# Performance work log

Hardware: AMD Instinct MI355X
Metric: run time of the kernel (lower is better)

The kernel has to match this reference:

```python
import jax, jax.numpy as jnp
import numpy as np

S = 10       # speakers (== num nodes N, per module construction)
D = 1024     # hidden_dim
R = 2 * S * S  # num_relations


def _forward(global_features, speaker, Wq, Wk, rgcn_weight, rgcn_root,
             rgcn_bias, gcn_rel_w, gcn_rel_b, gcn_root_w):
    N, d = global_features.shape
    # ---- single-head global attention -> edge weights (softmax over keys) ----
    # keys are the node features themselves (stacked N times in the original)
    q = global_features @ Wq                       # [N, D]
    k = global_features @ Wk                       # [N, D]
    attn = jax.nn.softmax((q @ k.T) / jnp.sqrt(jnp.asarray(d, q.dtype)), axis=-1)  # [N, N]

    # ---- dense all-pairs edge list, row-major (i, j) like itertools product ----
    src = jnp.repeat(jnp.arange(N), N)             # edge_index[0]
    dst = jnp.tile(jnp.arange(N), N)               # edge_index[1]
    edge_weight = attn.reshape(-1)                 # matches torch.flatten order

    # edge_type id = 2*(s_i*S + s_j) + direction, direction = 0 if i<j else 1
    etype = 2 * (speaker[src] * S + speaker[dst]) + (src >= dst).astype(speaker.dtype)

    # ---- RGCN with per-relation MEAN aggregation (PyG RGCNConv default) ----
    # mean is per (relation, dst-node) over weighted messages; transform is linear
    # so we fold weight[rel] into each edge and normalize by segment counts.
    seg = etype * N + dst                           # (relation, dst) segment id
    cnt = jax.ops.segment_sum(jnp.ones_like(edge_weight), seg, num_segments=R * N)
    w_e = edge_weight / cnt[seg]                    # cnt >= 1 on every live edge
    # per-edge gather of relation weight + matmul: [E, D] x [E, D, D] -> [E, D]
    msg = w_e[:, None] * jnp.einsum('ed,edf->ef', global_features[src], rgcn_weight[etype])
    out = jax.ops.segment_sum(msg, dst, num_segments=N)    # scatter-add to dst
    out = out + global_features @ rgcn_root + rgcn_bias    # root + bias

    # ---- GraphConv (sum aggregation, no edge weight): lin_rel(agg) + lin_root(x) ----
    agg = jax.ops.segment_sum(out[src], dst, num_segments=N)
    x2 = agg @ gcn_rel_w + gcn_rel_b + out @ gcn_root_w

    return jnp.concatenate([x2, global_features], axis=-1)  # [N, 2D]


def setup_inputs() -> dict:
    key = jax.random.key(0)
    ks = jax.random.split(key, 10)
    scale = 0.02
    return {
        'global_features': jax.random.normal(ks[0], (S, D), dtype=jnp.float32),
        'speaker': jax.random.randint(ks[1], (S,), 0, S, dtype=jnp.int32),
        'Wq': jax.random.normal(ks[2], (D, D), dtype=jnp.float32) * scale,
        'Wk': jax.random.normal(ks[3], (D, D), dtype=jnp.float32) * scale,
        'rgcn_weight': jax.random.normal(ks[4], (R, D, D), dtype=jnp.float32) * scale,
        'rgcn_root': jax.random.normal(ks[5], (D, D), dtype=jnp.float32) * scale,
        'rgcn_bias': jax.random.normal(ks[6], (D,), dtype=jnp.float32) * scale,
        'gcn_rel_w': jax.random.normal(ks[7], (D, D), dtype=jnp.float32) * scale,
        'gcn_rel_b': jax.random.normal(ks[8], (D,), dtype=jnp.float32) * scale,
        'gcn_root_w': jax.random.normal(ks[9], (D, D), dtype=jnp.float32) * scale,
    }


def reference(global_features, speaker, Wq, Wk, rgcn_weight, rgcn_root,
              rgcn_bias, gcn_rel_w, gcn_rel_b, gcn_root_w):
    return _forward(global_features, speaker, Wq, Wk, rgcn_weight, rgcn_root,
                    rgcn_bias, gcn_rel_w, gcn_rel_b, gcn_root_w)
```

## Files before the change

kernel.cpp:

```cpp
#include <hip/hip_runtime.h>

#define N 10
#define D 1024
#define NREL 200
#define KCH 32
#define KLEN 32
#define MAXG 8

typedef float f32x4 __attribute__((ext_vector_type(4)));

#define OFF_Q       0
#define OFF_K       (OFF_Q + N*D)
#define OFF_ROOT    (OFF_K + N*D)
#define OFF_X2ACC   (OFF_ROOT + N*D)
#define OFF_AGGREL  (OFF_X2ACC + N*D)
#define ZERO_FLOATS (OFF_AGGREL + D)
#define OFF_EM      ZERO_FLOATS
#define OFF_WE      (OFF_EM + N*N*D)
#define OFF_NITEMS  (OFF_WE + 128)
#define OFF_ITEMS   (OFF_NITEMS + 16)
#define OFF_EMPART  (OFF_ITEMS + 1024)

__global__ void build_groups(const int* __restrict__ speaker, int* __restrict__ n_items,
                             int* __restrict__ items) {
    __shared__ int sp[N];
    __shared__ int gcnt[NREL];
    __shared__ int ibase[NREL];
    int tid = threadIdx.x;
    if (tid < N) sp[tid] = speaker[tid];
    __syncthreads();
    if (tid < NREL) {
        int c = 0;
        for (int e = 0; e < N * N; ++e) {
            int src = e / N, dst = e % N;
            int et = 2 * (sp[src] * N + sp[dst]) + (src >= dst ? 1 : 0);
            c += (et == tid);
        }
        gcnt[tid] = c;
    }
    __syncthreads();
    if (tid == 0) {
        int b = 0;
        for (int t = 0; t < NREL; ++t) { ibase[t] = b; b += (gcnt[t] + MAXG - 1) / MAXG; }
        *n_items = b;
    }
    __syncthreads();
    if (tid < NREL && gcnt[tid] > 0) {
        int it = ibase[tid], slot = 0;
        int* rec = items + it * 10;
        for (int e = 0; e < N * N; ++e) {
            int src = e / N, dst = e % N;
            int et = 2 * (sp[src] * N + sp[dst]) + (src >= dst ? 1 : 0);
            if (et != tid) continue;
            if (slot == 0) rec[0] = tid;
            rec[2 + slot] = e;
            if (++slot == MAXG) { rec[1] = MAXG; ++it; rec = items + it * 10; slot = 0; }
        }
        if (slot > 0) { rec[1] = slot; for (int g = slot; g < MAXG; ++g) rec[2 + g] = -1; }
    }
}

__global__ void big_fused(const float* __restrict__ X, const float* __restrict__ Wrel,
                          const int* __restrict__ n_items, const int* __restrict__ items,
                          const float* __restrict__ Wq, const float* __restrict__ Wk,
                          const float* __restrict__ Wroot,
                          float* __restrict__ q, float* __restrict__ kout,
                          float* __restrict__ rootacc, float* __restrict__ em_part) {
    int bx = blockIdx.x, by = blockIdx.y, tid = threadIdx.x;
    if (bx < 100) {
        if (bx >= *n_items) return;
        __shared__ int   meta[10];
        __shared__ float xs[MAXG][KLEN];
        if (tid < 10) meta[tid] = items[bx * 10 + tid];
        __syncthreads();
        int t = meta[0], gsize = meta[1];
        {
            int g = tid >> 5, k = tid & 31;
            int e = meta[2 + g];
            xs[g][k] = (g < gsize) ? X[(e / N) * D + by * KLEN + k] : 0.f;
        }
        __syncthreads();
        int c0 = tid * 4;
        const float* W = Wrel + (size_t)t * D * D + (size_t)by * KLEN * D;
        f32x4 acc[MAXG];
#pragma unroll
        for (int g = 0; g < MAXG; ++g) acc[g] = 0.f;
#pragma unroll 4
        for (int k = 0; k < KLEN; ++k) {
            f32x4 w4 = *reinterpret_cast<const f32x4*>(W + (size_t)k * D + c0);
#pragma unroll
            for (int g = 0; g < MAXG; ++g) acc[g] += xs[g][k] * w4;
        }
        for (int g = 0; g < gsize; ++g) {
            *reinterpret_cast<f32x4*>(
                em_part + ((size_t)(by * (N * N) + meta[2 + g])) * D + c0) = acc[g];
        }
    } else {
        int sel = bx - 100;
        int kb  = (by & 7) * 128;
        int c   = (by >> 3) * 256 + tid;
        const float* W = (sel == 0) ? Wq : (sel == 1) ? Wk : Wroot;
        float*       Y = (sel == 0) ? q  : (sel == 1) ? kout : rootacc;
        __shared__ float xs2[N][128];
        for (int idx = tid; idx < N * 128; idx += 256) {
            int r = idx >> 7, k = idx & 127;
            xs2[r][k] = X[r * D + kb + k];
        }
        __syncthreads();
        float acc[N];
#pragma unroll
        for (int r = 0; r < N; ++r) acc[r] = 0.f;
#pragma unroll 4
        for (int k = 0; k < 128; ++k) {
            float w = W[(size_t)(kb + k) * D + c];
#pragma unroll
            for (int r = 0; r < N; ++r) acc[r] += xs2[r][k] * w;
        }
#pragma unroll
        for (int r = 0; r < N; ++r) atomicAdd(&Y[r * D + c], acc[r]);
    }
}

__global__ void reduce_em(const float* __restrict__ em_part, float* __restrict__ em) {
    __shared__ float ps[2][128];
    int e  = blockIdx.x;
    int c  = blockIdx.y * 128 + (threadIdx.x & 127);
    int h  = threadIdx.x >> 7;
    float s = 0.f;
#pragma unroll
    for (int i = 0; i < KCH / 2; ++i) {
        int by = h * (KCH / 2) + i;
        s += em_part[((size_t)(by * (N * N) + e)) * D + c];
    }
    ps[h][threadIdx.x & 127] = s;
    __syncthreads();
    if (threadIdx.x < 128) em[(size_t)e * D + c] = ps[0][threadIdx.x] + ps[1][threadIdx.x];
}

__global__ void attn_edges(const float* __restrict__ q, const float* __restrict__ k,
                           const int* __restrict__ speaker, float* __restrict__ w_e) {
    __shared__ float logits[N * N];
    __shared__ float attn[N * N];
    __shared__ int   cnt[NREL * N];
    int tid  = threadIdx.x;
    int wave = tid >> 6, lane = tid & 63;

    for (int p = wave; p < N * N; p += 16) {
        int i = p / N, j = p % N;
        const f32x4* qp = reinterpret_cast<const f32x4*>(q + i * D);
        const f32x4* kp = reinterpret_cast<const f32x4*>(k + j * D);
        float acc = 0.f;
#pragma unroll
        for (int it = 0; it < 4; ++it) {
            f32x4 qa = qp[lane + it * 64];
            f32x4 ka = kp[lane + it * 64];
            acc += qa.x * ka.x + qa.y * ka.y + qa.z * ka.z + qa.w * ka.w;
        }
        for (int off = 32; off; off >>= 1) acc += __shfl_down(acc, off);
        if (lane == 0) logits[p] = acc * (1.0f / 32.0f);
    }
    __syncthreads();

    if (tid < N) {
        float m = -1e30f;
        for (int j = 0; j < N; ++j) m = fmaxf(m, logits[tid * N + j]);
        float s = 0.f, e[N];
        for (int j = 0; j < N; ++j) { e[j] = expf(logits[tid * N + j] - m); s += e[j]; }
        for (int j = 0; j < N; ++j) attn[tid * N + j] = e[j] / s;
    }
    for (int i = tid; i < NREL * N; i += 1024) cnt[i] = 0;
    __syncthreads();

    int et = 0;
    if (tid < N * N) {
        int src = tid / N, dst = tid % N;
        et = 2 * (speaker[src] * N + speaker[dst]) + (src >= dst ? 1 : 0);
        atomicAdd(&cnt[et * N + dst], 1);
    }
    __syncthreads();

    if (tid < N * N) {
        w_e[tid] = attn[tid] / (float)cnt[et * N + (tid % N)];
    }
}

__global__ void combine_final(const float* __restrict__ em, const float* __restrict__ w_e,
                              const float* __restrict__ rootacc, const float* __restrict__ bias,
                              const float* __restrict__ root_w, const float* __restrict__ rel_w,
                              float* __restrict__ x2acc, float* __restrict__ aggrel) {
    __shared__ float wes[N * N];
    __shared__ float xs[128];
    int r   = blockIdx.x;
    int tid = threadIdx.x;
    int c   = blockIdx.y * 256 + tid;
    int kb  = blockIdx.z * 128;
    if (tid < N * N) wes[tid] = w_e[tid];
    __syncthreads();
    if (tid < 128) {
        int j = kb + tid;
        float v;
        if (r < N) {
            v = rootacc[r * D + j] + bias[j];
#pragma unroll
            for (int src = 0; src < N; ++src) {
                int e = src * N + r;
                v += wes[e] * em[(size_t)e * D + j];
            }
        } else {
            v = (float)N * bias[j];
#pragma unroll
            for (int rr = 0; rr < N; ++rr) v += rootacc[rr * D + j];
            for (int e = 0; e < N * N; ++e) v += wes[e] * em[(size_t)e * D + j];
        }
        xs[tid] = v;
    }
    __syncthreads();
    const float* W = (r < N) ? root_w : rel_w;
    float*       y = (r < N) ? x2acc + r * D : aggrel;
    const float* Wp = W + (size_t)kb * D + c;
    float acc = 0.f;
#pragma unroll 8
    for (int k = 0; k < 128; ++k) acc += xs[k] * Wp[(size_t)k * D];
    atomicAdd(&y[c], acc);
}

__global__ void final_concat(const float* __restrict__ x2acc, const float* __restrict__ aggrel,
                             const float* __restrict__ rel_b, const float* __restrict__ X,
                             float* __restrict__ dout) {
    int r = blockIdx.x, c = blockIdx.y * 256 + threadIdx.x;
    if (c < D) dout[r * 2 * D + c] = x2acc[r * D + c] + aggrel[c] + rel_b[c];
    else       dout[r * 2 * D + c] = X[r * D + (c - D)];
}

extern "C" void kernel_launch(void* const* d_in, const int* in_sizes, int n_in,
                              void* d_out, int out_size, void* d_ws, size_t ws_size,
                              hipStream_t stream) {
    const float* X          = (const float*)d_in[0];
    const int*   speaker    = (const int*)  d_in[1];
    const float* Wq         = (const float*)d_in[2];
    const float* Wk         = (const float*)d_in[3];
    const float* Wrel       = (const float*)d_in[4];
    const float* Wroot      = (const float*)d_in[5];
    const float* bias       = (const float*)d_in[6];
    const float* gcn_rel_w  = (const float*)d_in[7];
    const float* gcn_rel_b  = (const float*)d_in[8];
    const float* gcn_root_w = (const float*)d_in[9];
    float* ws   = (float*)d_ws;
    float* dout = (float*)d_out;

    float* q       = ws + OFF_Q;
    float* kbuf    = ws + OFF_K;
    float* rootacc = ws + OFF_ROOT;
    float* x2acc   = ws + OFF_X2ACC;
    float* aggrel  = ws + OFF_AGGREL;
    float* em      = ws + OFF_EM;
    float* w_e     = ws + OFF_WE;
    int*   nitems  = (int*)(ws + OFF_NITEMS);
    int*   items   = (int*)(ws + OFF_ITEMS);
    float* em_part = ws + OFF_EMPART;

    hipMemsetAsync(ws, 0, ZERO_FLOATS * sizeof(float), stream);

    dim3 blk(256);
    build_groups<<<1, blk, 0, stream>>>(speaker, nitems, items);

    big_fused<<<dim3(103, KCH), blk, 0, stream>>>(X, Wrel, nitems, items, Wq, Wk, Wroot,
                                                  q, kbuf, rootacc, em_part);

    attn_edges<<<1, dim3(1024), 0, stream>>>(q, kbuf, speaker, w_e);
    reduce_em<<<dim3(N * N, 8), blk, 0, stream>>>(em_part, em);
    combine_final<<<dim3(N + 1, 4, 8), blk, 0, stream>>>(em, w_e, rootacc, bias,
                                                         gcn_root_w, gcn_rel_w, x2acc, aggrel);
    final_concat<<<dim3(N, 8), blk, 0, stream>>>(x2acc, aggrel, gcn_rel_b, X, dout);
}
```

Before: 111.0 us.

## Fuse partial reduction into edge aggregation, restructure tail matvecs, replace memset

```diff
diff --git a/kernel.cpp b/kernel.cpp
--- a/kernel.cpp
+++ b/kernel.cpp
@@ -10,19 +10,26 @@
 typedef float f32x4 __attribute__((ext_vector_type(4)));
 
 #define OFF_Q       0
-#define OFF_K       (OFF_Q + N*D)
-#define OFF_ROOT    (OFF_K + N*D)
-#define OFF_X2ACC   (OFF_ROOT + N*D)
-#define OFF_AGGREL  (OFF_X2ACC + N*D)
-#define ZERO_FLOATS (OFF_AGGREL + D)
-#define OFF_EM      ZERO_FLOATS
-#define OFF_WE      (OFF_EM + N*N*D)
-#define OFF_NITEMS  (OFF_WE + 128)
-#define OFF_ITEMS   (OFF_NITEMS + 16)
-#define OFF_EMPART  (OFF_ITEMS + 1024)
-
-__global__ void build_groups(const int* __restrict__ speaker, int* __restrict__ n_items,
-                             int* __restrict__ items) {
+#define OFF_K       10240
+#define OFF_ROOT    20480
+#define OFF_X2ACC   30720
+#define OFF_AGGREL  40960
+#define OFF_AGG     41984
+#define ZERO_FLOATS 43008
+#define OFF_OUT     43008
+#define OFF_WE      53248
+#define OFF_NITEMS  53376
+#define OFF_ITEMS   53392
+#define OFF_EMPART  54400
+
+__global__ void build_zero(const int* __restrict__ speaker, int* __restrict__ n_items,
+                           int* __restrict__ items, float* __restrict__ wsz) {
+    if (blockIdx.x > 0) {
+        int base = (blockIdx.x - 1) * 1024 + threadIdx.x * 4;
+        f32x4 z = 0.f;
+        *reinterpret_cast<f32x4*>(wsz + base) = z;
+        return;
+    }
     __shared__ int sp[N];
     __shared__ int gcnt[NREL];
     __shared__ int ibase[NREL];
@@ -85,11 +92,16 @@
         f32x4 acc[MAXG];
 #pragma unroll
         for (int g = 0; g < MAXG; ++g) acc[g] = 0.f;
-#pragma unroll 4
-        for (int k = 0; k < KLEN; ++k) {
-            f32x4 w4 = *reinterpret_cast<const f32x4*>(W + (size_t)k * D + c0);
-#pragma unroll
-            for (int g = 0; g < MAXG; ++g) acc[g] += xs[g][k] * w4;
+        for (int kk = 0; kk < KLEN; kk += 8) {
+            f32x4 wb[8];
+#pragma unroll
+            for (int u = 0; u < 8; ++u)
+                wb[u] = *reinterpret_cast<const f32x4*>(W + (size_t)(kk + u) * D + c0);
+#pragma unroll
+            for (int u = 0; u < 8; ++u) {
+#pragma unroll
+                for (int g = 0; g < MAXG; ++g) acc[g] += xs[g][kk + u] * wb[u];
+            }
         }
         for (int g = 0; g < gsize; ++g) {
             *reinterpret_cast<f32x4*>(
@@ -121,22 +133,6 @@
     }
 }
 
-__global__ void reduce_em(const float* __restrict__ em_part, float* __restrict__ em) {
-    __shared__ float ps[2][128];
-    int e  = blockIdx.x;
-    int c  = blockIdx.y * 128 + (threadIdx.x & 127);
-    int h  = threadIdx.x >> 7;
-    float s = 0.f;
-#pragma unroll
-    for (int i = 0; i < KCH / 2; ++i) {
-        int by = h * (KCH / 2) + i;
-        s += em_part[((size_t)(by * (N * N) + e)) * D + c];
-    }
-    ps[h][threadIdx.x & 127] = s;
-    __syncthreads();
-    if (threadIdx.x < 128) em[(size_t)e * D + c] = ps[0][threadIdx.x] + ps[1][threadIdx.x];
-}
-
 __global__ void attn_edges(const float* __restrict__ q, const float* __restrict__ k,
                            const int* __restrict__ speaker, float* __restrict__ w_e) {
     __shared__ float logits[N * N];
@@ -184,52 +180,95 @@
     }
 }
 
-__global__ void combine_final(const float* __restrict__ em, const float* __restrict__ w_e,
-                              const float* __restrict__ rootacc, const float* __restrict__ bias,
-                              const float* __restrict__ root_w, const float* __restrict__ rel_w,
-                              float* __restrict__ x2acc, float* __restrict__ aggrel) {
+__global__ void e1_out(const float* __restrict__ em_part, const float* __restrict__ w_e,
+                       const float* __restrict__ rootacc, const float* __restrict__ bias,
+                       const float* __restrict__ X,
+                       float* __restrict__ out, float* __restrict__ agg,
+                       float* __restrict__ dout) {
     __shared__ float wes[N * N];
-    __shared__ float xs[128];
-    int r   = blockIdx.x;
+    __shared__ float red[8][128];
+    int dst = blockIdx.x, jt = blockIdx.y;
     int tid = threadIdx.x;
-    int c   = blockIdx.y * 256 + tid;
-    int kb  = blockIdx.z * 128;
+    int lane32 = tid & 31, g = tid >> 5;
+    int jbase = jt * 128;
     if (tid < N * N) wes[tid] = w_e[tid];
     __syncthreads();
+    f32x4 s = 0.f;
+    for (int p = 0; p < 40; ++p) {
+        int idx = p * 8 + g;
+        int by = idx / 10, src = idx % 10;
+        f32x4 v = *reinterpret_cast<const f32x4*>(
+            em_part + ((size_t)(by * (N * N) + src * N + dst)) * D + jbase + lane32 * 4);
+        s += wes[src * N + dst] * v;
+    }
+    *reinterpret_cast<f32x4*>(&red[g][lane32 * 4]) = s;
+    __syncthreads();
     if (tid < 128) {
-        int j = kb + tid;
-        float v;
-        if (r < N) {
-            v = rootacc[r * D + j] + bias[j];
-#pragma unroll
-            for (int src = 0; src < N; ++src) {
-                int e = src * N + r;
-                v += wes[e] * em[(size_t)e * D + j];
+        float t = 0.f;
+#pragma unroll
+        for (int gg = 0; gg < 8; ++gg) t += red[gg][tid];
+        int j = jbase + tid;
+        float o = t + rootacc[dst * D + j] + bias[j];
+        out[dst * D + j] = o;
+        atomicAdd(&agg[j], o);
+        dout[dst * 2 * D + D + j] = X[dst * D + j];
+    }
+}
+
+__global__ void e2_matvec(const float* __restrict__ out, const float* __restrict__ agg,
+                          const float* __restrict__ root_w, const float* __restrict__ rel_w,
+                          float* __restrict__ x2acc, float* __restrict__ aggrel) {
+    __shared__ float xs[N][32];
+    int kb  = blockIdx.x * 32;
+    int w   = blockIdx.y;
+    int tid = threadIdx.x;
+    int c0  = tid * 4;
+    if (w == 0) {
+        for (int i = tid; i < N * 32; i += 256)
+            xs[i >> 5][i & 31] = out[(i >> 5) * D + kb + (i & 31)];
+        __syncthreads();
+        f32x4 acc[N];
+#pragma unroll
+        for (int r = 0; r < N; ++r) acc[r] = 0.f;
+        for (int kk = 0; kk < 32; kk += 8) {
+            f32x4 wb[8];
+#pragma unroll
+            for (int u = 0; u < 8; ++u)
+                wb[u] = *reinterpret_cast<const f32x4*>(root_w + (size_t)(kb + kk + u) * D + c0);
+#pragma unroll
+            for (int u = 0; u < 8; ++u) {
+#pragma unroll
+                for (int r = 0; r < N; ++r) acc[r] += xs[r][kk + u] * wb[u];
             }
-        } else {
-            v = (float)N * bias[j];
-#pragma unroll
-            for (int rr = 0; rr < N; ++rr) v += rootacc[rr * D + j];
-            for (int e = 0; e < N * N; ++e) v += wes[e] * em[(size_t)e * D + j];
-        }
-        xs[tid] = v;
-    }
-    __syncthreads();
-    const float* W = (r < N) ? root_w : rel_w;
-    float*       y = (r < N) ? x2acc + r * D : aggrel;
-    const float* Wp = W + (size_t)kb * D + c;
-    float acc = 0.f;
-#pragma unroll 8
-    for (int k = 0; k < 128; ++k) acc += xs[k] * Wp[(size_t)k * D];
-    atomicAdd(&y[c], acc);
-}
-
-__global__ void final_concat(const float* __restrict__ x2acc, const float* __restrict__ aggrel,
-                             const float* __restrict__ rel_b, const float* __restrict__ X,
-                             float* __restrict__ dout) {
+        }
+#pragma unroll
+        for (int r = 0; r < N; ++r) {
+            float* y = x2acc + r * D + c0;
+            atomicAdd(y + 0, acc[r].x); atomicAdd(y + 1, acc[r].y);
+            atomicAdd(y + 2, acc[r].z); atomicAdd(y + 3, acc[r].w);
+        }
+    } else {
+        if (tid < 32) xs[0][tid] = agg[kb + tid];
+        __syncthreads();
+        f32x4 acc = 0.f;
+        for (int kk = 0; kk < 32; kk += 8) {
+            f32x4 wb[8];
+#pragma unroll
+            for (int u = 0; u < 8; ++u)
+                wb[u] = *reinterpret_cast<const f32x4*>(rel_w + (size_t)(kb + kk + u) * D + c0);
+#pragma unroll
+            for (int u = 0; u < 8; ++u) acc += xs[0][kk + u] * wb[u];
+        }
+        float* y = aggrel + c0;
+        atomicAdd(y + 0, acc.x); atomicAdd(y + 1, acc.y);
+        atomicAdd(y + 2, acc.z); atomicAdd(y + 3, acc.w);
+    }
+}
+
+__global__ void e3_concat(const float* __restrict__ x2acc, const float* __restrict__ aggrel,
+                          const float* __restrict__ rel_b, float* __restrict__ dout) {
     int r = blockIdx.x, c = blockIdx.y * 256 + threadIdx.x;
-    if (c < D) dout[r * 2 * D + c] = x2acc[r * D + c] + aggrel[c] + rel_b[c];
-    else       dout[r * 2 * D + c] = X[r * D + (c - D)];
+    dout[r * 2 * D + c] = x2acc[r * D + c] + aggrel[c] + rel_b[c];
 }
 
 extern "C" void kernel_launch(void* const* d_in, const int* in_sizes, int n_in,
@@ -253,23 +292,21 @@
     float* rootacc = ws + OFF_ROOT;
     float* x2acc   = ws + OFF_X2ACC;
     float* aggrel  = ws + OFF_AGGREL;
-    float* em      = ws + OFF_EM;
+    float* agg     = ws + OFF_AGG;
+    float* out     = ws + OFF_OUT;
     float* w_e     = ws + OFF_WE;
     int*   nitems  = (int*)(ws + OFF_NITEMS);
     int*   items   = (int*)(ws + OFF_ITEMS);
     float* em_part = ws + OFF_EMPART;
 
-    hipMemsetAsync(ws, 0, ZERO_FLOATS * sizeof(float), stream);
-
     dim3 blk(256);
-    build_groups<<<1, blk, 0, stream>>>(speaker, nitems, items);
+    build_zero<<<dim3(43), blk, 0, stream>>>(speaker, nitems, items, ws);
 
     big_fused<<<dim3(103, KCH), blk, 0, stream>>>(X, Wrel, nitems, items, Wq, Wk, Wroot,
                                                   q, kbuf, rootacc, em_part);
 
     attn_edges<<<1, dim3(1024), 0, stream>>>(q, kbuf, speaker, w_e);
-    reduce_em<<<dim3(N * N, 8), blk, 0, stream>>>(em_part, em);
-    combine_final<<<dim3(N + 1, 4, 8), blk, 0, stream>>>(em, w_e, rootacc, bias,
-                                                         gcn_root_w, gcn_rel_w, x2acc, aggrel);
-    final_concat<<<dim3(N, 8), blk, 0, stream>>>(x2acc, aggrel, gcn_rel_b, X, dout);
-}
+    e1_out<<<dim3(N, 8), blk, 0, stream>>>(em_part, w_e, rootacc, bias, X, out, agg, dout);
+    e2_matvec<<<dim3(32, 2), blk, 0, stream>>>(out, agg, gcn_root_w, gcn_rel_w, x2acc, aggrel);
+    e3_concat<<<dim3(N, 4), blk, 0, stream>>>(x2acc, aggrel, gcn_rel_b, dout);
+}
```

New measurement: 120.2 us. +8.3%, slower.
